# Optimization experiments

Measured on AMD Instinct MI355X. Metric: run time of the kernel, lower is better.

## Reference

```python
import jax, jax.numpy as jnp
import numpy as np

SEG = 512        # segment_size
DIL = 2          # dilation_rate
LN_EPS = 1e-5


def _layer_norm(x, gamma, beta):
    mu = jnp.mean(x, axis=-1, keepdims=True)
    var = jnp.var(x, axis=-1, keepdims=True)
    return (x - mu) * jax.lax.rsqrt(var + LN_EPS) * gamma + beta


def setup_inputs() -> dict:
    key = jax.random.key(0)
    ks = jax.random.split(key, 5)
    B, N, D = 4, 4096, 1024
    s = 0.02
    return {
        "x": jax.random.normal(ks[0], (B, N, D), dtype=jnp.float32),
        "Wq": jax.random.normal(ks[1], (D, D), dtype=jnp.float32) * s,
        "Wk": jax.random.normal(ks[2], (D, D), dtype=jnp.float32) * s,
        "Wv": jax.random.normal(ks[3], (D, D), dtype=jnp.float32) * s,
        "Wo": jax.random.normal(ks[4], (D, D), dtype=jnp.float32) * s,
        "gamma": jnp.ones((D,), dtype=jnp.float32),
        "beta": jnp.zeros((D,), dtype=jnp.float32),
    }


def reference(x, Wq, Wk, Wv, Wo, gamma, beta):
    B, N, D = x.shape
    n_seg = N // SEG
    s = SEG // DIL  # tokens per segment after dilation
    # strided dilated gather: [B, n_seg, s, D]
    xs = x.reshape(B, n_seg, SEG, D)[:, :, ::DIL, :]
    # torch Linear(bias=False): x @ W.T ; then LayerNorm on each of q,k,v
    q = _layer_norm(jnp.einsum('bgsd,ed->bgse', xs, Wq), gamma, beta)
    k = _layer_norm(jnp.einsum('bgsd,ed->bgse', xs, Wk), gamma, beta)
    v = _layer_norm(jnp.einsum('bgsd,ed->bgse', xs, Wv), gamma, beta)
    # causal SDPA with head_dim = D (no head split in the original code)
    scale = 1.0 / jnp.sqrt(jnp.asarray(D, dtype=q.dtype))
    scores = jnp.einsum('bgqd,bgkd->bgqk', q, k) * scale  # [B, n_seg, s, s]
    causal = jnp.tril(jnp.ones((s, s), dtype=bool))
    scores = jnp.where(causal, scores, jnp.finfo(scores.dtype).min)
    attn = jax.nn.softmax(scores, axis=-1)
    y = jnp.einsum('bgqk,bgkd->bgqd', attn, v)  # [B, n_seg, s, D]
    y = y.reshape(B, N // DIL, D)
    # strided scatter into zero-initialized full tensor
    y_full = jnp.zeros((B, N, D), dtype=y.dtype).at[:, ::DIL, :].set(y)
    out = jnp.einsum('bnd,ed->bne', y_full, Wo)
    return out
```

## Files before the change

kernel.cpp:

```cpp
#include <hip/hip_runtime.h>
#include <stdint.h>

typedef __bf16 bf16_t;
typedef __bf16 bf16x8 __attribute__((ext_vector_type(8)));
typedef __bf16 bf16x4 __attribute__((ext_vector_type(4)));
typedef float  f32x4  __attribute__((ext_vector_type(4)));


__device__ __forceinline__ void gload16(const void* g, void* lds)
{
    __builtin_amdgcn_global_load_lds(
        (__attribute__((address_space(1))) void*)(void*)g,
        (__attribute__((address_space(3))) void*)lds,
        16, 0, 0);
}

__device__ __forceinline__ f32x4 mfma16(bf16x8 a, bf16x8 b, f32x4 c)
{
    return __builtin_amdgcn_mfma_f32_16x16x32_bf16(a, b, c, 0, 0, 0);
}

#define SBAR()   asm volatile("s_barrier" ::: "memory")
#define LGKM0()  asm volatile("s_waitcnt lgkmcnt(0)" ::: "memory")
#define VMCNT(N) asm volatile("s_waitcnt vmcnt(" #N ")" ::: "memory")


__global__ __launch_bounds__(256)
void prep_kernel(const float* __restrict__ Wq, const float* __restrict__ Wk,
                 const float* __restrict__ Wv, const float* __restrict__ Wo,
                 const float* __restrict__ x,
                 bf16_t* __restrict__ Wqkv, bf16_t* __restrict__ Wob,
                 bf16_t* __restrict__ Xe)
{
    const int bid = blockIdx.x;
    const int t = threadIdx.x;
    if (bid < 4096) {
        const int which = bid >> 10;
        const int blk = bid & 1023;
        const float* src = which == 0 ? Wq : which == 1 ? Wk : which == 2 ? Wv : Wo;
        bf16_t* dst = which == 3 ? Wob : Wqkv + (size_t)which * 1048576;
        const size_t i = ((size_t)blk * 256 + t) * 4;
        float4 f = *(const float4*)&src[i];
        bf16x4 o;
        o[0] = (bf16_t)f.x; o[1] = (bf16_t)f.y; o[2] = (bf16_t)f.z; o[3] = (bf16_t)f.w;
        *(bf16x4*)&dst[i] = o;
    } else {
        const int m = bid - 4096;
        const int b = m >> 11, g = (m >> 8) & 7, j = m & 255;
        const float* src = x + ((size_t)b * 4096 + g * 512 + 2 * j) * 1024;
        bf16_t* dst = Xe + (size_t)m * 1024;
        float4 f = *(const float4*)&src[t * 4];
        bf16x4 o;
        o[0] = (bf16_t)f.x; o[1] = (bf16_t)f.y; o[2] = (bf16_t)f.z; o[3] = (bf16_t)f.w;
        *(bf16x4*)&dst[t * 4] = o;
    }
}

template<int EPI, int NSUB>
__global__ __launch_bounds__(512, 2)
void gemm_mt(const bf16_t* __restrict__ A, const bf16_t* __restrict__ B,
             void* __restrict__ Cv, int lda, int ldb, int ldc)
{
    __shared__ __align__(16) char lds[98304];

    const int tid = threadIdx.x;
    const int w = tid >> 6, lane = tid & 63;
    const int wr = w >> 2, wc = w & 3;
    const int fr = lane & 15, fg = lane >> 4;

    const int lin = blockIdx.y * 8 + blockIdx.x;
    const int L = (lin & 7) * 32 + (lin >> 3);
    const int bm = L >> 3, j = L & 7;
    const int NT = NSUB * 16;

    const int s = tid ^ ((tid >> 3) & 7);
    const char* srcA  = (const char*)A + ((size_t)(bm * 256 + (s >> 3)) * lda + (s & 7) * 8) * 2;
    const char* srcB0 = (const char*)B + ((size_t)(j * NSUB * 128 + (s >> 3)) * ldb + (s & 7) * 8) * 2;
    const size_t aStep  = (size_t)64 * lda * 2;
    const size_t bStep  = (size_t)64 * ldb * 2;
    const size_t bnStep = (size_t)128 * ldb * 2;
    const int ldsW = w * 1024;

#define STG_A(T, Q) gload16(srcA + (Q) * aStep + (size_t)((T) & 15) * 128,          \
                            lds + ((T) & 1) * 49152 + (Q) * 8192 + ldsW)
#define STG_B(T, U) gload16(srcB0 + (size_t)((T) >> 4) * bnStep + (U) * bStep       \
                                  + (size_t)((T) & 15) * 128,                        \
                            lds + ((T) & 1) * 49152 + 32768 + (U) * 8192 + ldsW)

    const int flip = (fr & 7) << 4;
    const int aoff = (wr * 128 + fr) * 128 + fg * 16;
    const int boff = 32768 + (wc * 32 + fr) * 128 + fg * 16;

    bf16x8 a[4][2], b[2][2];
    f32x4 acc[8][2] = {};

#define LDA(PH, CB) do {                                                        \
    _Pragma("unroll") for (int mi = 0; mi < 4; ++mi)                            \
    _Pragma("unroll") for (int ks = 0; ks < 2; ++ks)                            \
        a[mi][ks] = *(const bf16x8*)(lds + (CB) +                               \
            ((aoff + (PH) * 8192 + mi * 2048 + ks * 64) ^ flip));               \
} while (0)

#define LDB(CB) do {                                                            \
    _Pragma("unroll") for (int ni = 0; ni < 2; ++ni)                            \
    _Pragma("unroll") for (int ks = 0; ks < 2; ++ks)                            \
        b[ni][ks] = *(const bf16x8*)(lds + (CB) +                               \
            ((boff + ni * 2048 + ks * 64) ^ flip));                             \
} while (0)

#define MF(PH) do {                                                             \
    _Pragma("unroll") for (int mi = 0; mi < 4; ++mi)                            \
    _Pragma("unroll") for (int ni = 0; ni < 2; ++ni)                            \
    _Pragma("unroll") for (int ks = 0; ks < 2; ++ks)                            \
        acc[(PH) * 4 + mi][ni] =                                                \
            mfma16(b[ni][ks], a[mi][ks], acc[(PH) * 4 + mi][ni]);               \
} while (0)

    const int r0 = bm * 256 + wr * 128 + fr;
    const int c0w = wc * 32 + fg * 4;

#define DO_EPI(SUB) do {                                                                  \
    const int _c0 = (j * NSUB + (SUB)) * 128 + c0w;                                       \
    if constexpr (EPI == 0) {                                                             \
        bf16_t* C = (bf16_t*)Cv;                                                          \
        _Pragma("unroll") for (int mig = 0; mig < 8; ++mig)                               \
        _Pragma("unroll") for (int ni = 0; ni < 2; ++ni) {                                \
            const int row = r0 + (mig >> 2) * 64 + (mig & 3) * 16;                        \
            bf16x4 o;                                                                     \
            _Pragma("unroll") for (int r = 0; r < 4; ++r) o[r] = (bf16_t)acc[mig][ni][r]; \
            *(bf16x4*)&C[(size_t)row * ldc + _c0 + ni * 16] = o;                          \
        }                                                                                 \
    } else {                                                                              \
        float* C = (float*)Cv;                                                            \
        const f32x4 z4 = {0.f, 0.f, 0.f, 0.f};                                            \
        _Pragma("unroll") for (int mig = 0; mig < 8; ++mig)                               \
        _Pragma("unroll") for (int ni = 0; ni < 2; ++ni) {                                \
            const int m  = r0 + (mig >> 2) * 64 + (mig & 3) * 16;                         \
            const int gr = ((m >> 11) << 12) | (((m >> 8) & 7) << 9) | ((m & 255) << 1);  \
            *(f32x4*)&C[(size_t)gr * 1024 + _c0 + ni * 16]       = acc[mig][ni];          \
            *(f32x4*)&C[(size_t)(gr + 1) * 1024 + _c0 + ni * 16] = z4;                    \
        }                                                                                 \
    }                                                                                     \
    _Pragma("unroll") for (int mig = 0; mig < 8; ++mig)                                   \
    _Pragma("unroll") for (int ni = 0; ni < 2; ++ni)                                      \
        acc[mig][ni] = (f32x4){0.f, 0.f, 0.f, 0.f};                                       \
} while (0)

    STG_A(0, 0); STG_A(0, 1); STG_A(0, 2); STG_A(0, 3); STG_B(0, 0); STG_B(0, 1);
    STG_A(1, 0); STG_A(1, 2); STG_B(1, 0); STG_B(1, 1);
    VMCNT(4);
    SBAR();

    for (int t = 0; t < NT - 2; ++t) {
        const int cb = (t & 1) * 49152;
        LDA(0, cb); LDB(cb);
        STG_A(t + 1, 1); STG_A(t + 1, 3);
        SBAR(); LGKM0();
        __builtin_amdgcn_s_setprio(1); MF(0); __builtin_amdgcn_s_setprio(0);
        VMCNT(6);
        SBAR();
        LDA(1, cb);
        STG_A(t + 2, 0); STG_A(t + 2, 2); STG_B(t + 2, 0); STG_B(t + 2, 1);
        SBAR(); LGKM0();
        __builtin_amdgcn_s_setprio(1); MF(1); __builtin_amdgcn_s_setprio(0);
        VMCNT(6);
        if ((t & 15) == 15) DO_EPI(t >> 4);
        SBAR();
    }

    {
        const int cb = ((NT - 2) & 1) * 49152;
        LDA(0, cb); LDB(cb);
        STG_A(NT - 1, 1); STG_A(NT - 1, 3);
        SBAR(); LGKM0();
        MF(0);
        VMCNT(6);
        SBAR();
        LDA(1, cb);
        SBAR(); LGKM0();
        MF(1);
        VMCNT(0);
        SBAR();
    }
    {
        const int cb = ((NT - 1) & 1) * 49152;
        LDA(0, cb); LDB(cb);
        LGKM0();
        MF(0);
        LDA(1, cb);
        LGKM0();
        MF(1);
    }
    DO_EPI(NSUB - 1);

#undef STG_A
#undef STG_B
#undef LDA
#undef LDB
#undef MF
#undef DO_EPI
}

template<int EPI>
__global__ __launch_bounds__(256)
void gemm_nt(const bf16_t* __restrict__ A, const bf16_t* __restrict__ B,
             void* __restrict__ Cv,
             int K, int lda, int ldb, int ldc,
             long sA, long sB, long sC, int flags)
{
    __shared__ __align__(16) bf16_t Asm[128 * 32];
    __shared__ __align__(16) bf16_t Bsm[128 * 32];

    const int bn = blockIdx.x, bm = blockIdx.y, bz = blockIdx.z;
    const int tid  = threadIdx.x;
    const int wave = tid >> 6;
    const int lane = tid & 63;
    const int wr = wave >> 1, wc = wave & 1;

    const bf16_t* Ab = A + (long)bz * sA;
    const bf16_t* Bb = B + (long)bz * sB;

    const int Keff = ((flags & 1) && bm == 0) ? (K >> 1) : K;

    const int sw0 = tid ^ ((tid >> 3) & 3);
    const int dd1 = tid + 256;
    const int sw1 = dd1 ^ ((dd1 >> 3) & 3);
    const bf16_t* a0 = Ab + (size_t)(bm * 128 + (sw0 >> 2)) * lda + (sw0 & 3) * 8;
    const bf16_t* a1 = Ab + (size_t)(bm * 128 + (sw1 >> 2)) * lda + (sw1 & 3) * 8;
    const bf16_t* b0 = Bb + (size_t)(bn * 128 + (sw0 >> 2)) * ldb + (sw0 & 3) * 8;
    const bf16_t* b1 = Bb + (size_t)(bn * 128 + (sw1 >> 2)) * ldb + (sw1 & 3) * 8;
    char* ldsA = (char*)Asm + wave * 1024;
    char* ldsB = (char*)Bsm + wave * 1024;

    f32x4 acc[4][4] = {};

    const int frow = lane & 15;
    const int fk   = (lane >> 4) * 8;
    const int flip = (frow & 6) << 2;

    for (int k0 = 0; k0 < Keff; k0 += 32) {
        gload16(a0, ldsA);
        gload16(a1, ldsA + 4096);
        gload16(b0, ldsB);
        gload16(b1, ldsB + 4096);
        a0 += 32; a1 += 32; b0 += 32; b1 += 32;
        __syncthreads();

        bf16x8 af[4], bfr[4];
#pragma unroll
        for (int mi = 0; mi < 4; ++mi)
            af[mi] = *(const bf16x8*)&Asm[(size_t)(((wr * 64 + mi * 16 + frow) * 32 + fk) ^ flip)];
#pragma unroll
        for (int ni = 0; ni < 4; ++ni)
            bfr[ni] = *(const bf16x8*)&Bsm[(size_t)(((wc * 64 + ni * 16 + frow) * 32 + fk) ^ flip)];
#pragma unroll
        for (int mi = 0; mi < 4; ++mi)
#pragma unroll
            for (int ni = 0; ni < 4; ++ni)
                acc[mi][ni] = mfma16(bfr[ni], af[mi], acc[mi][ni]);
        __syncthreads();
    }

    const int row0 = bm * 128 + wr * 64 + frow;
    const int col0 = bn * 128 + wc * 64 + (lane >> 4) * 4;

    if constexpr (EPI == 0) {
        bf16_t* C = (bf16_t*)Cv + (long)bz * sC;
#pragma unroll
        for (int mi = 0; mi < 4; ++mi)
#pragma unroll
            for (int ni = 0; ni < 4; ++ni) {
                bf16x4 o;
#pragma unroll
                for (int r = 0; r < 4; ++r) o[r] = (bf16_t)acc[mi][ni][r];
                *(bf16x4*)&C[(size_t)(row0 + mi * 16) * ldc + col0 + ni * 16] = o;
            }
    } else {
        float* C = (float*)Cv + (long)bz * sC;
#pragma unroll
        for (int mi = 0; mi < 4; ++mi)
#pragma unroll
            for (int ni = 0; ni < 4; ++ni)
                *(f32x4*)&C[(size_t)(row0 + mi * 16) * ldc + col0 + ni * 16] = acc[mi][ni];
    }
}

template<int NI>
__device__ __forceinline__ void qk_block(
    const bf16_t* __restrict__ Ab, const bf16_t* __restrict__ Bb,
    bf16_t* __restrict__ Pseg, int qb, char* smem, int tid)
{
    bf16_t* Asm = (bf16_t*)smem;
    bf16_t* Bsm = (bf16_t*)(smem + 8192);
    float*  red = (float*)(smem + 24576);

    const int w = tid >> 6, lane = tid & 63;
    const int wr = w >> 2, wc = w & 3;
    const int frow = lane & 15, fg = lane >> 4;

    const int g0 = tid, g1 = tid + 512;
    const int s0 = g0 ^ ((g0 >> 3) & 3);
    const int s1 = g1 ^ ((g1 >> 3) & 3);
    const bf16_t* a0 = Ab + (size_t)(s0 >> 2) * 3072 + (s0 & 3) * 8;
    const bf16_t* b0 = Bb + (size_t)(s0 >> 2) * 3072 + (s0 & 3) * 8;
    const bf16_t* b1 = Bb + (size_t)(s1 >> 2) * 3072 + (s1 & 3) * 8;
    char* ldsA = smem + w * 1024;
    char* ldsB = smem + 8192 + w * 1024;

    f32x4 acc[4][NI] = {};
    const int fk = fg * 8;
    const int flip = (frow & 6) << 2;
    const int Nw = NI * 16;

    for (int k0 = 0; k0 < 1024; k0 += 32) {
        gload16(a0, ldsA);
        gload16(b0, ldsB);
        if (NI == 4) gload16(b1, ldsB + 8192);
        a0 += 32; b0 += 32; b1 += 32;
        __syncthreads();

        bf16x8 af[4], bf_[NI];
#pragma unroll
        for (int mi = 0; mi < 4; ++mi)
            af[mi] = *(const bf16x8*)&Asm[((wr * 64 + mi * 16 + frow) * 32 + fk) ^ flip];
#pragma unroll
        for (int ni = 0; ni < NI; ++ni)
            bf_[ni] = *(const bf16x8*)&Bsm[((wc * Nw + ni * 16 + frow) * 32 + fk) ^ flip];
#pragma unroll
        for (int mi = 0; mi < 4; ++mi)
#pragma unroll
            for (int ni = 0; ni < NI; ++ni)
                acc[mi][ni] = mfma16(bf_[ni], af[mi], acc[mi][ni]);
        __syncthreads();
    }

    const int base_rloc = wr * 64 + frow;
    const float scale = 1.0f / 32.0f;

#pragma unroll
    for (int mi = 0; mi < 4; ++mi) {
        const int rl = base_rloc + mi * 16;
        const int grow = qb * 128 + rl;
        float m = -3.0e38f;
#pragma unroll
        for (int ni = 0; ni < NI; ++ni)
#pragma unroll
            for (int r = 0; r < 4; ++r) {
                const int col = wc * Nw + ni * 16 + fg * 4 + r;
                float v = acc[mi][ni][r] * scale;
                if (col > grow) v = -3.0e38f;
                acc[mi][ni][r] = v;
                m = fmaxf(m, v);
            }
        m = fmaxf(m, __shfl_xor(m, 16));
        m = fmaxf(m, __shfl_xor(m, 32));
        if (fg == 0) red[rl * 4 + wc] = m;
    }
    __syncthreads();
    float mx[4];
#pragma unroll
    for (int mi = 0; mi < 4; ++mi) {
        const int rl = base_rloc + mi * 16;
        mx[mi] = fmaxf(fmaxf(red[rl * 4 + 0], red[rl * 4 + 1]),
                       fmaxf(red[rl * 4 + 2], red[rl * 4 + 3]));
    }
    __syncthreads();

#pragma unroll
    for (int mi = 0; mi < 4; ++mi) {
        const int rl = base_rloc + mi * 16;
        float s = 0.f;
#pragma unroll
        for (int ni = 0; ni < NI; ++ni)
#pragma unroll
            for (int r = 0; r < 4; ++r) {
                const float e = __expf(acc[mi][ni][r] - mx[mi]);
                acc[mi][ni][r] = e;
                s += e;
            }
        s += __shfl_xor(s, 16);
        s += __shfl_xor(s, 32);
        if (fg == 0) red[rl * 4 + wc] = s;
    }
    __syncthreads();

#pragma unroll
    for (int mi = 0; mi < 4; ++mi) {
        const int rl = base_rloc + mi * 16;
        const float inv = 1.0f / (red[rl * 4 + 0] + red[rl * 4 + 1] +
                                  red[rl * 4 + 2] + red[rl * 4 + 3]);
        const int grow = qb * 128 + rl;
#pragma unroll
        for (int ni = 0; ni < NI; ++ni) {
            bf16x4 o;
#pragma unroll
            for (int r = 0; r < 4; ++r) o[r] = (bf16_t)(acc[mi][ni][r] * inv);
            *(bf16x4*)&Pseg[(size_t)grow * 256 + wc * Nw + ni * 16 + fg * 4] = o;
        }
    }
}

__global__ __launch_bounds__(512)
void qk_sm_tr_kernel(const bf16_t* __restrict__ qkv, bf16_t* __restrict__ P,
                     bf16_t* __restrict__ Vt)
{
    __shared__ __align__(16) char smem[26624];
    const int bid = blockIdx.x;
    const int tid = threadIdx.x;

    if (bid < 64) {
        const int seg = bid >> 1, qb = bid & 1;
        const bf16_t* Ab = qkv + (size_t)seg * 786432 + (size_t)qb * 128 * 3072;
        const bf16_t* Bb = qkv + (size_t)seg * 786432 + 1024;
        bf16_t* Pseg = P + (size_t)seg * 65536;
        if (qb) qk_block<4>(Ab, Bb, Pseg, 1, smem, tid);
        else    qk_block<2>(Ab, Bb, Pseg, 0, smem, tid);
    } else {
        const int id2 = bid - 64;
        const int seg = id2 >> 6;
        const int rem = id2 & 63;
        const int eb = rem >> 2, kb = rem & 3;
        bf16_t* tile = (bf16_t*)smem;
        const int rr = tid >> 3, cs = (tid & 7) * 8;
        const bf16_t* src = qkv + ((size_t)seg * 256 + kb * 64 + rr) * 3072
                                + 2048 + eb * 64 + cs;
        bf16x8 v = *(const bf16x8*)src;
#pragma unroll
        for (int i = 0; i < 8; ++i) tile[rr * 65 + cs + i] = v[i];
        __syncthreads();
        bf16x8 o;
#pragma unroll
        for (int i = 0; i < 8; ++i) o[i] = tile[(cs + i) * 65 + rr];
        *(bf16x8*)&Vt[(size_t)seg * 262144 + (size_t)(eb * 64 + rr) * 256 + kb * 64 + cs] = o;
    }
}

__global__ __launch_bounds__(256)
void ln_kernel(bf16_t* __restrict__ qkv,
               const float* __restrict__ gamma, const float* __restrict__ beta)
{
    const int t = threadIdx.x;
    const int r = t >> 7;
    const int row = blockIdx.x * 2 + r;
    const int which = blockIdx.y;
    bf16_t* p = qkv + (size_t)row * 3072 + which * 1024;
    const int li = t & 127;
    const int c0 = li * 8;

    bf16x8 v = *(const bf16x8*)&p[c0];
    float f[8];
    float s = 0.f, ss = 0.f;
#pragma unroll
    for (int i = 0; i < 8; ++i) { f[i] = (float)v[i]; s += f[i]; ss += f[i] * f[i]; }
#pragma unroll
    for (int o = 32; o; o >>= 1) { s += __shfl_xor(s, o); ss += __shfl_xor(ss, o); }

    __shared__ float rs_[4], rss_[4];
    const int wave = t >> 6, lane = t & 63;
    if (lane == 0) { rs_[wave] = s; rss_[wave] = ss; }
    __syncthreads();
    s  = rs_[2 * r] + rs_[2 * r + 1];
    ss = rss_[2 * r] + rss_[2 * r + 1];

    const float mu   = s * (1.f / 1024.f);
    const float var  = ss * (1.f / 1024.f) - mu * mu;
    const float rstd = rsqrtf(var + 1e-5f);

    bf16x8 o;
#pragma unroll
    for (int i = 0; i < 8; ++i)
        o[i] = (bf16_t)((f[i] - mu) * rstd * gamma[c0 + i] + beta[c0 + i]);
    *(bf16x8*)&p[c0] = o;
}


extern "C" void kernel_launch(void* const* d_in, const int* in_sizes, int n_in,
                              void* d_out, int out_size, void* d_ws, size_t ws_size,
                              hipStream_t stream)
{
    const float* x     = (const float*)d_in[0];
    const float* Wq    = (const float*)d_in[1];
    const float* Wk    = (const float*)d_in[2];
    const float* Wv    = (const float*)d_in[3];
    const float* Wo    = (const float*)d_in[4];
    const float* gamma = (const float*)d_in[5];
    const float* beta  = (const float*)d_in[6];
    float* out = (float*)d_out;

    char* ws = (char*)d_ws;
    bf16_t* Xe   = (bf16_t*)(ws);
    bf16_t* Wqkv = (bf16_t*)(ws + (16u  << 20));
    bf16_t* Wob  = (bf16_t*)(ws + (22u  << 20));
    bf16_t* QKV  = (bf16_t*)(ws + (24u  << 20));
    bf16_t* P    = (bf16_t*)(ws + (80u  << 20));
    bf16_t* Vt   = (bf16_t*)(ws + (84u  << 20));
    bf16_t* Y    = (bf16_t*)(ws + (100u << 20));

    prep_kernel<<<12288, 256, 0, stream>>>(Wq, Wk, Wv, Wo, x, Wqkv, Wob, Xe);

    gemm_mt<0, 3><<<dim3(8, 32), 512, 0, stream>>>(
        Xe, Wqkv, QKV, 1024, 1024, 3072);

    ln_kernel<<<dim3(4096, 3), 256, 0, stream>>>(QKV, gamma, beta);

    qk_sm_tr_kernel<<<64 + 2048, 512, 0, stream>>>(QKV, P, Vt);

    gemm_nt<0><<<dim3(8, 2, 32), 256, 0, stream>>>(
        P, Vt, Y, 256, 256, 256, 1024,
        65536L, 262144L, 262144L, 1);

    gemm_mt<2, 1><<<dim3(8, 32), 512, 0, stream>>>(
        Y, Wob, out, 1024, 1024, 1024);
}
```

Before: 171.9 us.

## Halve GEMM K-tile to cut LDS and raise occupancy to four blocks

The multi-tile GEMM's K step drops from 64 to 32, which halves the LDS footprint from 96KB to 48KB. Launch bounds now request four 512-thread blocks per CU instead of two. Staging is reorganised into A-low/A-high/B loads, with matching swizzle, offsets and wait counts, and only one k-slice of register fragments is kept. The aim is more resident waves to hide memory latency, at the cost of twice as many loop iterations and barriers and a tighter register budget.

```diff
diff --git a/kernel.cpp b/kernel.cpp
--- a/kernel.cpp
+++ b/kernel.cpp
@@ -57,11 +57,11 @@
 }
 
 template<int EPI, int NSUB>
-__global__ __launch_bounds__(512, 2)
+__global__ __launch_bounds__(512, 4)
 void gemm_mt(const bf16_t* __restrict__ A, const bf16_t* __restrict__ B,
              void* __restrict__ Cv, int lda, int ldb, int ldc)
 {
-    __shared__ __align__(16) char lds[98304];
+    __shared__ __align__(16) char lds[49152];
 
     const int tid = threadIdx.x;
     const int w = tid >> 6, lane = tid & 63;
@@ -71,49 +71,46 @@
     const int lin = blockIdx.y * 8 + blockIdx.x;
     const int L = (lin & 7) * 32 + (lin >> 3);
     const int bm = L >> 3, j = L & 7;
-    const int NT = NSUB * 16;
+    const int NT = NSUB * 32;
 
     const int s = tid ^ ((tid >> 3) & 7);
-    const char* srcA  = (const char*)A + ((size_t)(bm * 256 + (s >> 3)) * lda + (s & 7) * 8) * 2;
-    const char* srcB0 = (const char*)B + ((size_t)(j * NSUB * 128 + (s >> 3)) * ldb + (s & 7) * 8) * 2;
-    const size_t aStep  = (size_t)64 * lda * 2;
-    const size_t bStep  = (size_t)64 * ldb * 2;
+    const char* srcA  = (const char*)A + ((size_t)(bm * 256 + (s >> 2)) * lda + (s & 3) * 8) * 2;
+    const char* srcB0 = (const char*)B + ((size_t)(j * NSUB * 128 + (s >> 2)) * ldb + (s & 3) * 8) * 2;
+    const size_t aHalf  = (size_t)128 * lda * 2;
     const size_t bnStep = (size_t)128 * ldb * 2;
     const int ldsW = w * 1024;
 
-#define STG_A(T, Q) gload16(srcA + (Q) * aStep + (size_t)((T) & 15) * 128,          \
-                            lds + ((T) & 1) * 49152 + (Q) * 8192 + ldsW)
-#define STG_B(T, U) gload16(srcB0 + (size_t)((T) >> 4) * bnStep + (U) * bStep       \
-                                  + (size_t)((T) & 15) * 128,                        \
-                            lds + ((T) & 1) * 49152 + 32768 + (U) * 8192 + ldsW)
-
-    const int flip = (fr & 7) << 4;
-    const int aoff = (wr * 128 + fr) * 128 + fg * 16;
-    const int boff = 32768 + (wc * 32 + fr) * 128 + fg * 16;
-
-    bf16x8 a[4][2], b[2][2];
+#define STG_AL(T) gload16(srcA + (size_t)((T) & 31) * 64,                          \
+                          lds + ((T) & 1) * 24576 + ldsW)
+#define STG_AH(T) gload16(srcA + aHalf + (size_t)((T) & 31) * 64,                  \
+                          lds + ((T) & 1) * 24576 + 8192 + ldsW)
+#define STG_B(T)  gload16(srcB0 + (size_t)((T) >> 5) * bnStep + (size_t)((T) & 31) * 64, \
+                          lds + ((T) & 1) * 24576 + 16384 + ldsW)
+
+    const int flip = ((fr >> 1) & 7) << 4;
+    const int aoff = wr * 8192 + fr * 64 + fg * 16;
+    const int boff = 16384 + wc * 2048 + fr * 64 + fg * 16;
+
+    bf16x8 a[4], b[2];
     f32x4 acc[8][2] = {};
 
 #define LDA(PH, CB) do {                                                        \
     _Pragma("unroll") for (int mi = 0; mi < 4; ++mi)                            \
-    _Pragma("unroll") for (int ks = 0; ks < 2; ++ks)                            \
-        a[mi][ks] = *(const bf16x8*)(lds + (CB) +                               \
-            ((aoff + (PH) * 8192 + mi * 2048 + ks * 64) ^ flip));               \
+        a[mi] = *(const bf16x8*)(lds + (CB) +                                   \
+            ((aoff + (PH) * 4096 + mi * 1024) ^ flip));                         \
 } while (0)
 
 #define LDB(CB) do {                                                            \
     _Pragma("unroll") for (int ni = 0; ni < 2; ++ni)                            \
-    _Pragma("unroll") for (int ks = 0; ks < 2; ++ks)                            \
-        b[ni][ks] = *(const bf16x8*)(lds + (CB) +                               \
-            ((boff + ni * 2048 + ks * 64) ^ flip));                             \
+        b[ni] = *(const bf16x8*)(lds + (CB) +                                   \
+            ((boff + ni * 1024) ^ flip));                                       \
 } while (0)
 
 #define MF(PH) do {                                                             \
     _Pragma("unroll") for (int mi = 0; mi < 4; ++mi)                            \
     _Pragma("unroll") for (int ni = 0; ni < 2; ++ni)                            \
-    _Pragma("unroll") for (int ks = 0; ks < 2; ++ks)                            \
         acc[(PH) * 4 + mi][ni] =                                                \
-            mfma16(b[ni][ks], a[mi][ks], acc[(PH) * 4 + mi][ni]);               \
+            mfma16(b[ni], a[mi], acc[(PH) * 4 + mi][ni]);                       \
 } while (0)
 
     const int r0 = bm * 256 + wr * 128 + fr;
@@ -146,35 +143,35 @@
         acc[mig][ni] = (f32x4){0.f, 0.f, 0.f, 0.f};                                       \
 } while (0)
 
-    STG_A(0, 0); STG_A(0, 1); STG_A(0, 2); STG_A(0, 3); STG_B(0, 0); STG_B(0, 1);
-    STG_A(1, 0); STG_A(1, 2); STG_B(1, 0); STG_B(1, 1);
-    VMCNT(4);
+    STG_AL(0); STG_AH(0); STG_B(0);
+    STG_B(1);
+    VMCNT(1);
     SBAR();
 
-    for (int t = 0; t < NT - 2; ++t) {
-        const int cb = (t & 1) * 49152;
+    for (int t = 0; t <= NT - 3; ++t) {
+        const int cb = (t & 1) * 24576;
         LDA(0, cb); LDB(cb);
-        STG_A(t + 1, 1); STG_A(t + 1, 3);
+        STG_AL(t + 1); STG_AH(t + 1);
         SBAR(); LGKM0();
         __builtin_amdgcn_s_setprio(1); MF(0); __builtin_amdgcn_s_setprio(0);
-        VMCNT(6);
+        VMCNT(3);
         SBAR();
         LDA(1, cb);
-        STG_A(t + 2, 0); STG_A(t + 2, 2); STG_B(t + 2, 0); STG_B(t + 2, 1);
+        STG_B(t + 2);
         SBAR(); LGKM0();
         __builtin_amdgcn_s_setprio(1); MF(1); __builtin_amdgcn_s_setprio(0);
-        VMCNT(6);
-        if ((t & 15) == 15) DO_EPI(t >> 4);
+        VMCNT(1);
+        if ((t & 31) == 31) DO_EPI(t >> 5);
         SBAR();
     }
 
     {
-        const int cb = ((NT - 2) & 1) * 49152;
+        const int cb = ((NT - 2) & 1) * 24576;
         LDA(0, cb); LDB(cb);
-        STG_A(NT - 1, 1); STG_A(NT - 1, 3);
+        STG_AL(NT - 1); STG_AH(NT - 1);
         SBAR(); LGKM0();
         MF(0);
-        VMCNT(6);
+        VMCNT(3);
         SBAR();
         LDA(1, cb);
         SBAR(); LGKM0();
@@ -183,7 +180,7 @@
         SBAR();
     }
     {
-        const int cb = ((NT - 1) & 1) * 49152;
+        const int cb = ((NT - 1) & 1) * 24576;
         LDA(0, cb); LDB(cb);
         LGKM0();
         MF(0);
@@ -193,7 +190,8 @@
     }
     DO_EPI(NSUB - 1);
 
-#undef STG_A
+#undef STG_AL
+#undef STG_AH
 #undef STG_B
 #undef LDA
 #undef LDB
```

Result: slower. 179.0 us (+4.1%).
